# Optimization experiments

Hardware: AMD Instinct MI355X
Metric: run time of the kernel (lower is better)

Reference implementation:

```python
import jax, jax.numpy as jnp
import numpy as np
import math

V, E, R, B, T, L = 32000, 256, 1024, 64, 2048, 3
EPS = 1e-5


def setup_inputs() -> dict:
    key = jax.random.key(0)
    ks = jax.random.split(key, 8)
    x = jax.random.randint(ks[0], (B, T), 0, V)
    embed_w = jax.random.normal(ks[1], (V, E), jnp.float32)
    Win0 = jax.random.normal(ks[2], (E, R), jnp.float32) / math.sqrt(E) / 0.9
    Win1 = jax.random.normal(ks[3], (R, R), jnp.float32) / math.sqrt(R) / 0.9
    Win2 = jax.random.normal(ks[4], (R, R), jnp.float32) / math.sqrt(R) / 0.9
    R0 = jax.random.normal(ks[5], (R, R), jnp.float32) / math.sqrt(R) / 0.9
    R1 = jax.random.normal(ks[6], (R, R), jnp.float32) / math.sqrt(R) / 0.9
    R2 = jax.random.normal(ks[7], (R, R), jnp.float32) / math.sqrt(R) / 0.9
    ln_w = jnp.ones((R,), jnp.float32)
    ln_b = jnp.zeros((R,), jnp.float32)
    return dict(x=x, embed_w=embed_w, Win0=Win0, Win1=Win1, Win2=Win2,
                R0=R0, R1=R1, R2=R2, ln_w=ln_w, ln_b=ln_b)


def reference(x, embed_w, Win0, Win1, Win2, R0, R1, R2, ln_w, ln_b):
    Wins = (Win0, Win1, Win2)
    Rs = (R0, R1, R2)
    x_embed = embed_w[x]                        # [B, T, E]
    b = x.shape[0]
    rsz = R0.shape[0]
    init = tuple(jnp.zeros((b, rsz), x_embed.dtype) for _ in range(L))

    def step(states, xt):                       # xt: [B, E]
        cur = xt
        new = []
        for i in range(L):                      # 'deep': layer i>0 consumes states[i-1] (fresh)
            s = jnp.tanh(states[i] @ Rs[i] + cur @ Wins[i])
            new.append(s)
            cur = s
        return tuple(new), None

    states, _ = jax.lax.scan(step, init, jnp.swapaxes(x_embed, 0, 1))  # scan over T
    h = states[-1]                              # [B, R]
    mu = jnp.mean(h, axis=-1, keepdims=True)
    var = jnp.var(h, axis=-1, keepdims=True)
    return (h - mu) / jnp.sqrt(var + EPS) * ln_w + ln_b
```

## Files before the change

### kernel.cpp

```cpp
#include <hip/hip_runtime.h>

#define VV    32000
#define EE    256
#define RSZ   1024
#define BB    64
#define TT    2048
#define NGRP  3
#define EPSLN 1e-5f

#define NBLK_PER_GRP 64
#define NBLK  (NBLK_PER_GRP * NGRP)
#define NTHR  512
#define SLAB  (BB * RSZ)

#define BAR_OFF (NGRP * 2 * SLAB)

__device__ __forceinline__ void fma_step4x4(const float4 (&b)[4], const float* wrow,
                                            float (&acc)[4][4]) {
#pragma unroll
    for (int j = 0; j < 4; ++j) {
        const float4 w = *reinterpret_cast<const float4*>(wrow + j * 16);
#pragma unroll
        for (int r = 0; r < 4; ++r) {
            const float a = reinterpret_cast<const float*>(&b[r])[j];
            acc[r][0] = fmaf(a, w.x, acc[r][0]);
            acc[r][1] = fmaf(a, w.y, acc[r][1]);
            acc[r][2] = fmaf(a, w.z, acc[r][2]);
            acc[r][3] = fmaf(a, w.w, acc[r][3]);
        }
    }
}

template<int NSTEPS>
__device__ __forceinline__ void dot_stream(const float* const (&p)[4],
                                           const float* w, float (&acc)[4][4]) {
    float4 ring[4][4];
    constexpr int PRO = (NSTEPS < 4) ? NSTEPS : 4;
#pragma unroll
    for (int s = 0; s < PRO; ++s)
#pragma unroll
        for (int r = 0; r < 4; ++r)
            ring[s][r] = *reinterpret_cast<const float4*>(p[r] + s * 4);

    constexpr int MAIN = NSTEPS - PRO;
#pragma unroll
    for (int j = 0; j < MAIN; ++j) {
        fma_step4x4(ring[j & 3], w + j * 64, acc);
#pragma unroll
        for (int r = 0; r < 4; ++r)
            ring[j & 3][r] = *reinterpret_cast<const float4*>(p[r] + (j + 4) * 4);
    }
#pragma unroll
    for (int j = MAIN; j < NSTEPS; ++j)
        fma_step4x4(ring[j & 3], w + j * 64, acc);
}

__global__ __launch_bounds__(NTHR, 2)
void reservoir_main(const int*   __restrict__ x,
                    const float* __restrict__ embed_w,
                    const float* __restrict__ Win0,
                    const float* __restrict__ Win1,
                    const float* __restrict__ Win2,
                    const float* __restrict__ Rm0,
                    const float* __restrict__ Rm1,
                    const float* __restrict__ Rm2,
                    const float* __restrict__ ln_w,
                    const float* __restrict__ ln_b,
                    float*       __restrict__ states,
                    unsigned*    __restrict__ bar,
                    float*       __restrict__ out)
{
    const int blk   = blockIdx.x;
    const int grp   = blk >> 6;
    const int gb    = blk & 63;
    const int c0    = gb << 4;
    const int tid   = threadIdx.x;
    const int kg    = tid >> 6;
    const int idx   = tid & 63;
    const int rbase = (idx >> 2) << 2;
    const int cg4   = (idx & 3) << 2;

    const float* Wl  = (grp == 0) ? Win0 : ((grp == 1) ? Win1 : Win2);
    const float* Rl  = (grp == 0) ? Rm0  : ((grp == 1) ? Rm1  : Rm2);
    const int    Kw  = (grp == 0) ? EE : RSZ;
    const int    Kw8 = Kw >> 3;

    __shared__ float wlds[2048 * 16];
    __shared__ float pbuf[8][32][20];

    for (int i = tid; i < RSZ * 16; i += NTHR) {
        const int k = i >> 4, c = i & 15;
        wlds[i] = Rl[(size_t)k * RSZ + c0 + c];
    }
    for (int i = tid; i < Kw * 16; i += NTHR) {
        const int k = i >> 4, c = i & 15;
        wlds[RSZ * 16 + i] = Wl[(size_t)k * RSZ + c0 + c];
    }
    __syncthreads();

    unsigned* leaf  = bar;
    unsigned* root  = bar + 128;
    unsigned* epoch = bar + 160;

    float* const sl = states + (size_t)grp * 2 * SLAB;
    const float* const wRb = wlds + (kg << 7) * 16 + cg4;
    const float* const wWb = wlds + (RSZ + kg * Kw8) * 16 + cg4;

    int xidx[4];
    if (grp == 0) {
#pragma unroll
        for (int r = 0; r < 4; ++r) xidx[r] = x[(rbase + r) * TT + 0];
    }

    for (int tick = 0; tick < TT + NGRP - 1; ++tick) {
        const int t = tick - grp;
        if (0 <= t && t < TT) {
            const float* sprev = sl + (size_t)((t + 1) & 1) * SLAB;

            float acc[4][4];
#pragma unroll
            for (int r = 0; r < 4; ++r)
#pragma unroll
                for (int c = 0; c < 4; ++c) acc[r][c] = 0.f;

            {
                const float* aR[4];
#pragma unroll
                for (int r = 0; r < 4; ++r)
                    aR[r] = sprev + (size_t)(rbase + r) * RSZ + (kg << 7);
                dot_stream<32>(aR, wRb, acc);
            }
            {
                const float* aW[4];
                if (grp == 0) {
#pragma unroll
                    for (int r = 0; r < 4; ++r)
                        aW[r] = embed_w + (size_t)xidx[r] * EE + kg * Kw8;
                    dot_stream<8>(aW, wWb, acc);
                } else {
                    const float* cb = states + ((size_t)(grp - 1) * 2 + (t & 1)) * SLAB;
#pragma unroll
                    for (int r = 0; r < 4; ++r)
                        aW[r] = cb + (size_t)(rbase + r) * RSZ + kg * Kw8;
                    dot_stream<32>(aW, wWb, acc);
                }
            }

            if (grp == 0 && t + 1 < TT) {
#pragma unroll
                for (int r = 0; r < 4; ++r) xidx[r] = x[(rbase + r) * TT + t + 1];
            }

            float* sout = sl + (size_t)(t & 1) * SLAB;

            if (idx < 32) {
#pragma unroll
                for (int r = 0; r < 4; ++r) {
                    const int row = rbase + r;
                    *reinterpret_cast<float4*>(&pbuf[kg][row][cg4 ^ ((row & 3) << 2)])
                        = make_float4(acc[r][0], acc[r][1], acc[r][2], acc[r][3]);
                }
            }
            __syncthreads();
            {
                const int row = tid >> 4, col = tid & 15;
                const int cw  = ((col & 12) ^ ((row & 3) << 2)) | (col & 3);
                float s = 0.f;
#pragma unroll
                for (int g = 0; g < 8; ++g) s += pbuf[g][row][cw];
                sout[(size_t)row * RSZ + c0 + col] = tanhf(s);
            }
            __syncthreads();
            if (idx >= 32) {
#pragma unroll
                for (int r = 0; r < 4; ++r) {
                    const int row = rbase + r, rl = row & 31;
                    *reinterpret_cast<float4*>(&pbuf[kg][rl][cg4 ^ ((rl & 3) << 2)])
                        = make_float4(acc[r][0], acc[r][1], acc[r][2], acc[r][3]);
                }
            }
            __syncthreads();
            {
                const int rl = tid >> 4, col = tid & 15;
                const int cw = ((col & 12) ^ ((rl & 3) << 2)) | (col & 3);
                float s = 0.f;
#pragma unroll
                for (int g = 0; g < 8; ++g) s += pbuf[g][rl][cw];
                sout[(size_t)(32 + rl) * RSZ + c0 + col] = tanhf(s);
            }
        }

        __syncthreads();
        if (tid == 0) {
            __threadfence();
            const unsigned target = (unsigned)(tick + 1);
            unsigned prev = atomicAdd(&leaf[(blk & 7) << 4], 1u);
            if (prev == 24u * target - 1u) {
                prev = atomicAdd(root, 1u);
                if (prev == 8u * target - 1u)
                    __hip_atomic_store(epoch, target, __ATOMIC_RELEASE,
                                       __HIP_MEMORY_SCOPE_AGENT);
            }
            while (__hip_atomic_load(epoch, __ATOMIC_RELAXED,
                                     __HIP_MEMORY_SCOPE_AGENT) < target)
                __builtin_amdgcn_s_sleep(2);
            __threadfence();
        }
        __syncthreads();
    }

    if (blk < BB) {
        const float* h = states + ((size_t)2 * 2 + 1) * SLAB + (size_t)blk * RSZ;
        float* red = &pbuf[0][0][0];

        const float hv0 = h[tid];
        const float hv1 = h[tid + 512];
        float v = hv0 + hv1;
#pragma unroll
        for (int o = 32; o > 0; o >>= 1) v += __shfl_down(v, o, 64);
        if ((tid & 63) == 0) red[tid >> 6] = v;
        __syncthreads();
        if (tid == 0) {
            float s = 0.f;
#pragma unroll
            for (int i = 0; i < 8; ++i) s += red[i];
            red[20] = s / (float)RSZ;
        }
        __syncthreads();
        const float mu = red[20];
        const float d0 = hv0 - mu, d1 = hv1 - mu;
        v = d0 * d0 + d1 * d1;
#pragma unroll
        for (int o = 32; o > 0; o >>= 1) v += __shfl_down(v, o, 64);
        __syncthreads();
        if ((tid & 63) == 0) red[tid >> 6] = v;
        __syncthreads();
        if (tid == 0) {
            float s = 0.f;
#pragma unroll
            for (int i = 0; i < 8; ++i) s += red[i];
            red[21] = rsqrtf(s / (float)RSZ + EPSLN);
        }
        __syncthreads();
        const float inv = red[21];
        out[blk * RSZ + tid]       = d0 * inv * ln_w[tid]       + ln_b[tid];
        out[blk * RSZ + tid + 512] = d1 * inv * ln_w[tid + 512] + ln_b[tid + 512];
    }
}

extern "C" void kernel_launch(void* const* d_in, const int* in_sizes, int n_in,
                              void* d_out, int out_size, void* d_ws, size_t ws_size,
                              hipStream_t stream) {
    const int*   x       = (const int*)  d_in[0];
    const float* embed_w = (const float*)d_in[1];
    const float* Win0    = (const float*)d_in[2];
    const float* Win1    = (const float*)d_in[3];
    const float* Win2    = (const float*)d_in[4];
    const float* Rm0     = (const float*)d_in[5];
    const float* Rm1     = (const float*)d_in[6];
    const float* Rm2     = (const float*)d_in[7];
    const float* ln_w    = (const float*)d_in[8];
    const float* ln_b    = (const float*)d_in[9];
    float*       out     = (float*)d_out;
    float*       states  = (float*)d_ws;
    unsigned*    bar     = (unsigned*)((float*)d_ws + BAR_OFF);

    hipMemsetAsync(d_ws, 0, (size_t)BAR_OFF * sizeof(float) + 4096, stream);

    void* args[] = {
        (void*)&x, (void*)&embed_w,
        (void*)&Win0, (void*)&Win1, (void*)&Win2,
        (void*)&Rm0, (void*)&Rm1, (void*)&Rm2,
        (void*)&ln_w, (void*)&ln_b,
        (void*)&states, (void*)&bar, (void*)&out
    };
    hipLaunchCooperativeKernel(reinterpret_cast<void*>(reservoir_main),
                               dim3(NBLK), dim3(NTHR), args, 0, stream);
}
```

Measured before the change: 61.33 ms.

## Stage state rows into LDS via async global_load_lds triple-buffered pipeline

Replaces the per-thread register-ring global loads of previous-state and input rows with asynchronous global_load_lds copies into a triple-buffered, swizzled LDS staging area, with barriers between chunks. It also changes the thread mapping: 4 k-groups by 2 row-halves with 2 rows per thread, instead of 8 k-groups with 4 rows per thread. Each row chunk is then loaded once per block and shared across waves, which cuts redundant global/L2 traffic. The cost is a workgroup barrier per 32-wide chunk, plus more LDS use that may affect the two-blocks-per-CU occupancy.

```diff
diff --git a/kernel.cpp b/kernel.cpp
--- a/kernel.cpp
+++ b/kernel.cpp
@@ -15,45 +15,15 @@
 
 #define BAR_OFF (NGRP * 2 * SLAB)
 
-__device__ __forceinline__ void fma_step4x4(const float4 (&b)[4], const float* wrow,
-                                            float (&acc)[4][4]) {
-#pragma unroll
-    for (int j = 0; j < 4; ++j) {
-        const float4 w = *reinterpret_cast<const float4*>(wrow + j * 16);
-#pragma unroll
-        for (int r = 0; r < 4; ++r) {
-            const float a = reinterpret_cast<const float*>(&b[r])[j];
-            acc[r][0] = fmaf(a, w.x, acc[r][0]);
-            acc[r][1] = fmaf(a, w.y, acc[r][1]);
-            acc[r][2] = fmaf(a, w.z, acc[r][2]);
-            acc[r][3] = fmaf(a, w.w, acc[r][3]);
-        }
-    }
-}
-
-template<int NSTEPS>
-__device__ __forceinline__ void dot_stream(const float* const (&p)[4],
-                                           const float* w, float (&acc)[4][4]) {
-    float4 ring[4][4];
-    constexpr int PRO = (NSTEPS < 4) ? NSTEPS : 4;
-#pragma unroll
-    for (int s = 0; s < PRO; ++s)
-#pragma unroll
-        for (int r = 0; r < 4; ++r)
-            ring[s][r] = *reinterpret_cast<const float4*>(p[r] + s * 4);
-
-    constexpr int MAIN = NSTEPS - PRO;
-#pragma unroll
-    for (int j = 0; j < MAIN; ++j) {
-        fma_step4x4(ring[j & 3], w + j * 64, acc);
-#pragma unroll
-        for (int r = 0; r < 4; ++r)
-            ring[j & 3][r] = *reinterpret_cast<const float4*>(p[r] + (j + 4) * 4);
-    }
-#pragma unroll
-    for (int j = MAIN; j < NSTEPS; ++j)
-        fma_step4x4(ring[j & 3], w + j * 64, acc);
-}
+#define WOFF   0
+#define STAGE  (2048 * 16)
+#define CHUNKF (64 * 32)
+#define SMEMF  (STAGE + 3 * CHUNKF)
+
+typedef __attribute__((address_space(1))) const void gas_cvoid;
+typedef __attribute__((address_space(3))) void las_void;
+
+#define SCHED_FENCE() asm volatile("" ::: "memory")
 
 __global__ __launch_bounds__(NTHR, 2)
 void reservoir_main(const int*   __restrict__ x,
@@ -70,31 +40,39 @@
                     unsigned*    __restrict__ bar,
                     float*       __restrict__ out)
 {
-    const int blk   = blockIdx.x;
-    const int grp   = blk >> 6;
-    const int gb    = blk & 63;
-    const int c0    = gb << 4;
-    const int tid   = threadIdx.x;
-    const int kg    = tid >> 6;
-    const int idx   = tid & 63;
-    const int rbase = (idx >> 2) << 2;
-    const int cg4   = (idx & 3) << 2;
-
-    const float* Wl  = (grp == 0) ? Win0 : ((grp == 1) ? Win1 : Win2);
-    const float* Rl  = (grp == 0) ? Rm0  : ((grp == 1) ? Rm1  : Rm2);
-    const int    Kw  = (grp == 0) ? EE : RSZ;
-    const int    Kw8 = Kw >> 3;
-
-    __shared__ float wlds[2048 * 16];
-    __shared__ float pbuf[8][32][20];
+    const int blk  = blockIdx.x;
+    const int grp  = blk >> 6;
+    const int gb   = blk & 63;
+    const int c0   = gb << 4;
+    const int tid  = threadIdx.x;
+    const int wv   = tid >> 6;
+    const int lane = tid & 63;
+    const int kg   = wv & 3;
+    const int rh   = wv >> 2;
+    const int row0 = (rh << 5) + ((lane >> 2) << 1);
+    const int row1 = row0 + 1;
+    const int cg4  = (lane & 3) << 2;
+    const int sw0  = (row0 >> 1) & 7;
+    const int sw1  = (row1 >> 1) & 7;
+
+    const int srow = (wv << 3) + (lane >> 3);
+    const int sko  = lane & 7;
+    const int sswz = ((sko ^ ((srow >> 1) & 7)) << 2);
+
+    const float* Wl = (grp == 0) ? Win0 : ((grp == 1) ? Win1 : Win2);
+    const float* Rl = (grp == 0) ? Rm0  : ((grp == 1) ? Rm1  : Rm2);
+    const int Kw    = (grp == 0) ? EE : RSZ;
+    const int nCh   = 32 + (Kw >> 5);
+
+    __shared__ float smem[SMEMF];
 
     for (int i = tid; i < RSZ * 16; i += NTHR) {
         const int k = i >> 4, c = i & 15;
-        wlds[i] = Rl[(size_t)k * RSZ + c0 + c];
+        smem[WOFF + i] = Rl[(size_t)k * RSZ + c0 + c];
     }
     for (int i = tid; i < Kw * 16; i += NTHR) {
         const int k = i >> 4, c = i & 15;
-        wlds[RSZ * 16 + i] = Wl[(size_t)k * RSZ + c0 + c];
+        smem[WOFF + RSZ * 16 + i] = Wl[(size_t)k * RSZ + c0 + c];
     }
     __syncthreads();
 
@@ -103,89 +81,105 @@
     unsigned* epoch = bar + 160;
 
     float* const sl = states + (size_t)grp * 2 * SLAB;
-    const float* const wRb = wlds + (kg << 7) * 16 + cg4;
-    const float* const wWb = wlds + (RSZ + kg * Kw8) * 16 + cg4;
-
-    int xidx[4];
-    if (grp == 0) {
-#pragma unroll
-        for (int r = 0; r < 4; ++r) xidx[r] = x[(rbase + r) * TT + 0];
-    }
 
     for (int tick = 0; tick < TT + NGRP - 1; ++tick) {
         const int t = tick - grp;
         if (0 <= t && t < TT) {
             const float* sprev = sl + (size_t)((t + 1) & 1) * SLAB;
-
-            float acc[4][4];
-#pragma unroll
-            for (int r = 0; r < 4; ++r)
-#pragma unroll
-                for (int c = 0; c < 4; ++c) acc[r][c] = 0.f;
-
-            {
-                const float* aR[4];
-#pragma unroll
-                for (int r = 0; r < 4; ++r)
-                    aR[r] = sprev + (size_t)(rbase + r) * RSZ + (kg << 7);
-                dot_stream<32>(aR, wRb, acc);
-            }
-            {
-                const float* aW[4];
-                if (grp == 0) {
-#pragma unroll
-                    for (int r = 0; r < 4; ++r)
-                        aW[r] = embed_w + (size_t)xidx[r] * EE + kg * Kw8;
-                    dot_stream<8>(aW, wWb, acc);
-                } else {
-                    const float* cb = states + ((size_t)(grp - 1) * 2 + (t & 1)) * SLAB;
-#pragma unroll
-                    for (int r = 0; r < 4; ++r)
-                        aW[r] = cb + (size_t)(rbase + r) * RSZ + kg * Kw8;
-                    dot_stream<32>(aW, wWb, acc);
+            const float* gR = sprev + (size_t)srow * RSZ + sswz;
+            const float* gW;
+            if (grp == 0) {
+                const int tok = x[srow * TT + t];
+                gW = embed_w + (size_t)tok * EE + sswz;
+            } else {
+                gW = states + ((size_t)(grp - 1) * 2 + (t & 1)) * SLAB
+                     + (size_t)srow * RSZ + sswz;
+            }
+            asm volatile("s_waitcnt vmcnt(0)" ::: "memory");
+
+            float acc[2][4] = {{0.f,0.f,0.f,0.f},{0.f,0.f,0.f,0.f}};
+
+            auto ISSUE = [&](int c) {
+                const float* g = (c < 32) ? (gR + (c << 5)) : (gW + ((c - 32) << 5));
+                float* l = &smem[STAGE + (c % 3) * CHUNKF + (wv << 8)];
+                __builtin_amdgcn_global_load_lds((gas_cvoid*)g, (las_void*)l, 16, 0, 0);
+            };
+            auto COMPUTE = [&](int c) {
+                const int sb = STAGE + (c % 3) * CHUNKF;
+                const int wk = (c < 32) ? (c << 5) : (RSZ + ((c - 32) << 5));
+                const int wb = WOFF + (wk + (kg << 3)) * 16 + cg4;
+#pragma unroll
+                for (int s = 0; s < 2; ++s) {
+                    const int kol = (kg << 1) + s;
+                    const float4 a0 = *(const float4*)&smem[sb + row0 * 32 + ((kol ^ sw0) << 2)];
+                    const float4 a1 = *(const float4*)&smem[sb + row1 * 32 + ((kol ^ sw1) << 2)];
+#pragma unroll
+                    for (int j = 0; j < 4; ++j) {
+                        const float4 w = *(const float4*)&smem[wb + ((s << 2) + j) * 16];
+                        const float e0 = ((const float*)&a0)[j];
+                        const float e1 = ((const float*)&a1)[j];
+                        acc[0][0] = fmaf(e0, w.x, acc[0][0]);
+                        acc[0][1] = fmaf(e0, w.y, acc[0][1]);
+                        acc[0][2] = fmaf(e0, w.z, acc[0][2]);
+                        acc[0][3] = fmaf(e0, w.w, acc[0][3]);
+                        acc[1][0] = fmaf(e1, w.x, acc[1][0]);
+                        acc[1][1] = fmaf(e1, w.y, acc[1][1]);
+                        acc[1][2] = fmaf(e1, w.z, acc[1][2]);
+                        acc[1][3] = fmaf(e1, w.w, acc[1][3]);
+                    }
                 }
-            }
-
-            if (grp == 0 && t + 1 < TT) {
-#pragma unroll
-                for (int r = 0; r < 4; ++r) xidx[r] = x[(rbase + r) * TT + t + 1];
+            };
+
+            ISSUE(0);
+            ISSUE(1);
+            asm volatile("s_waitcnt vmcnt(1)" ::: "memory");
+            __builtin_amdgcn_s_barrier();
+            SCHED_FENCE();
+
+            for (int c = 0; c < nCh; ++c) {
+                if (c + 2 < nCh) ISSUE(c + 2);
+                COMPUTE(c);
+                if (c + 2 < nCh) {
+                    asm volatile("s_waitcnt vmcnt(1)" ::: "memory");
+                } else if (c + 1 < nCh) {
+                    asm volatile("s_waitcnt vmcnt(0)" ::: "memory");
+                }
+                __builtin_amdgcn_s_barrier();
+                SCHED_FENCE();
             }
 
             float* sout = sl + (size_t)(t & 1) * SLAB;
 
-            if (idx < 32) {
-#pragma unroll
-                for (int r = 0; r < 4; ++r) {
-                    const int row = rbase + r;
-                    *reinterpret_cast<float4*>(&pbuf[kg][row][cg4 ^ ((row & 3) << 2)])
-                        = make_float4(acc[r][0], acc[r][1], acc[r][2], acc[r][3]);
-                }
+            if (wv < 4) {
+                *(float4*)&smem[STAGE + ((kg << 5) + row0) * 20 + (cg4 ^ ((row0 & 3) << 2))]
+                    = make_float4(acc[0][0], acc[0][1], acc[0][2], acc[0][3]);
+                *(float4*)&smem[STAGE + ((kg << 5) + row1) * 20 + (cg4 ^ ((row1 & 3) << 2))]
+                    = make_float4(acc[1][0], acc[1][1], acc[1][2], acc[1][3]);
             }
             __syncthreads();
             {
                 const int row = tid >> 4, col = tid & 15;
-                const int cw  = ((col & 12) ^ ((row & 3) << 2)) | (col & 3);
+                const int cw  = (((col & 12) ^ ((row & 3) << 2)) | (col & 3));
                 float s = 0.f;
 #pragma unroll
-                for (int g = 0; g < 8; ++g) s += pbuf[g][row][cw];
+                for (int g = 0; g < 4; ++g) s += smem[STAGE + ((g << 5) + row) * 20 + cw];
                 sout[(size_t)row * RSZ + c0 + col] = tanhf(s);
             }
             __syncthreads();
-            if (idx >= 32) {
-#pragma unroll
-                for (int r = 0; r < 4; ++r) {
-                    const int row = rbase + r, rl = row & 31;
-                    *reinterpret_cast<float4*>(&pbuf[kg][rl][cg4 ^ ((rl & 3) << 2)])
-                        = make_float4(acc[r][0], acc[r][1], acc[r][2], acc[r][3]);
-                }
+            if (wv >= 4) {
+                const int rl0 = row0 & 31, rl1 = row1 & 31;
+                *(float4*)&smem[STAGE + ((kg << 5) + rl0) * 20 + (cg4 ^ ((rl0 & 3) << 2))]
+                    = make_float4(acc[0][0], acc[0][1], acc[0][2], acc[0][3]);
+                *(float4*)&smem[STAGE + ((kg << 5) + rl1) * 20 + (cg4 ^ ((rl1 & 3) << 2))]
+                    = make_float4(acc[1][0], acc[1][1], acc[1][2], acc[1][3]);
             }
             __syncthreads();
             {
                 const int rl = tid >> 4, col = tid & 15;
-                const int cw = ((col & 12) ^ ((rl & 3) << 2)) | (col & 3);
+                const int cw = (((col & 12) ^ ((rl & 3) << 2)) | (col & 3));
                 float s = 0.f;
 #pragma unroll
-                for (int g = 0; g < 8; ++g) s += pbuf[g][rl][cw];
+                for (int g = 0; g < 4; ++g) s += smem[STAGE + ((g << 5) + rl) * 20 + cw];
                 sout[(size_t)(32 + rl) * RSZ + c0 + col] = tanhf(s);
             }
         }
@@ -211,7 +205,7 @@
 
     if (blk < BB) {
         const float* h = states + ((size_t)2 * 2 + 1) * SLAB + (size_t)blk * RSZ;
-        float* red = &pbuf[0][0][0];
+        float* red = &smem[STAGE];
 
         const float hv0 = h[tid];
         const float hv1 = h[tid + 512];
```

Result: slower. 89.96 ms (+46.7%).

## Use 8x4 register tiles with 16-way K split and double-buffered loads

Applied to the files above, without the earlier changes.

Each thread now computes 8 batch rows by 4 columns over a K slice half as long, split 16 ways instead of 8. This doubles reuse of each LDS weight float4 across rows and replaces the 4-deep load ring with a two-buffer A/B scheme. The partial-sum reduction now runs in four 16-row phases with 16 partials each, and launch bounds drop to one block per SM to leave room for the extra registers. The cost is more barriers per step, a longer reduction, and a risk of register pressure or stalls from less load pipelining.

```diff
diff --git a/kernel.cpp b/kernel.cpp
--- a/kernel.cpp
+++ b/kernel.cpp
@@ -15,13 +15,13 @@
 
 #define BAR_OFF (NGRP * 2 * SLAB)
 
-__device__ __forceinline__ void fma_step4x4(const float4 (&b)[4], const float* wrow,
-                                            float (&acc)[4][4]) {
+__device__ __forceinline__ void fma_step8x4(const float4 (&b)[8], const float* wrow,
+                                            float (&acc)[8][4]) {
 #pragma unroll
     for (int j = 0; j < 4; ++j) {
         const float4 w = *reinterpret_cast<const float4*>(wrow + j * 16);
 #pragma unroll
-        for (int r = 0; r < 4; ++r) {
+        for (int r = 0; r < 8; ++r) {
             const float a = reinterpret_cast<const float*>(&b[r])[j];
             acc[r][0] = fmaf(a, w.x, acc[r][0]);
             acc[r][1] = fmaf(a, w.y, acc[r][1]);
@@ -31,31 +31,30 @@
     }
 }
 
+__device__ __forceinline__ void ld8(float4 (&b)[8], const float* const (&p)[8],
+                                    int off) {
+#pragma unroll
+    for (int r = 0; r < 8; ++r)
+        b[r] = *reinterpret_cast<const float4*>(p[r] + off);
+}
+
 template<int NSTEPS>
-__device__ __forceinline__ void dot_stream(const float* const (&p)[4],
-                                           const float* w, float (&acc)[4][4]) {
-    float4 ring[4][4];
-    constexpr int PRO = (NSTEPS < 4) ? NSTEPS : 4;
-#pragma unroll
-    for (int s = 0; s < PRO; ++s)
-#pragma unroll
-        for (int r = 0; r < 4; ++r)
-            ring[s][r] = *reinterpret_cast<const float4*>(p[r] + s * 4);
-
-    constexpr int MAIN = NSTEPS - PRO;
-#pragma unroll
-    for (int j = 0; j < MAIN; ++j) {
-        fma_step4x4(ring[j & 3], w + j * 64, acc);
-#pragma unroll
-        for (int r = 0; r < 4; ++r)
-            ring[j & 3][r] = *reinterpret_cast<const float4*>(p[r] + (j + 4) * 4);
-    }
-#pragma unroll
-    for (int j = MAIN; j < NSTEPS; ++j)
-        fma_step4x4(ring[j & 3], w + j * 64, acc);
-}
-
-__global__ __launch_bounds__(NTHR, 2)
+__device__ __forceinline__ void dot8(const float* const (&p)[8],
+                                     const float* w, float (&acc)[8][4]) {
+    float4 A[8], B[8];
+    ld8(A, p, 0);
+    ld8(B, p, 4);
+    for (int j = 0; j < NSTEPS - 2; j += 2) {
+        fma_step8x4(A, w + j * 64, acc);
+        ld8(A, p, (j + 2) * 4);
+        fma_step8x4(B, w + (j + 1) * 64, acc);
+        ld8(B, p, (j + 3) * 4);
+    }
+    fma_step8x4(A, w + (NSTEPS - 2) * 64, acc);
+    fma_step8x4(B, w + (NSTEPS - 1) * 64, acc);
+}
+
+__global__ __launch_bounds__(NTHR, 1)
 void reservoir_main(const int*   __restrict__ x,
                     const float* __restrict__ embed_w,
                     const float* __restrict__ Win0,
@@ -75,18 +74,19 @@
     const int gb    = blk & 63;
     const int c0    = gb << 4;
     const int tid   = threadIdx.x;
-    const int kg    = tid >> 6;
-    const int idx   = tid & 63;
-    const int rbase = (idx >> 2) << 2;
+    const int kg    = tid >> 5;
+    const int idx   = tid & 31;
+    const int rbase = (idx >> 2) << 3;
     const int cg4   = (idx & 3) << 2;
+    const int ph    = rbase >> 4;
 
     const float* Wl  = (grp == 0) ? Win0 : ((grp == 1) ? Win1 : Win2);
     const float* Rl  = (grp == 0) ? Rm0  : ((grp == 1) ? Rm1  : Rm2);
     const int    Kw  = (grp == 0) ? EE : RSZ;
-    const int    Kw8 = Kw >> 3;
+    const int    KwS = Kw >> 4;
 
     __shared__ float wlds[2048 * 16];
-    __shared__ float pbuf[8][32][20];
+    __shared__ float pbuf[16][16][20];
 
     for (int i = tid; i < RSZ * 16; i += NTHR) {
         const int k = i >> 4, c = i & 15;
@@ -103,13 +103,13 @@
     unsigned* epoch = bar + 160;
 
     float* const sl = states + (size_t)grp * 2 * SLAB;
-    const float* const wRb = wlds + (kg << 7) * 16 + cg4;
-    const float* const wWb = wlds + (RSZ + kg * Kw8) * 16 + cg4;
-
-    int xidx[4];
+    const float* const wRb = wlds + (kg << 6) * 16 + cg4;
+    const float* const wWb = wlds + (RSZ + kg * KwS) * 16 + cg4;
+
+    int xidx[8];
     if (grp == 0) {
 #pragma unroll
-        for (int r = 0; r < 4; ++r) xidx[r] = x[(rbase + r) * TT + 0];
+        for (int r = 0; r < 8; ++r) xidx[r] = x[(rbase + r) * TT + 0];
     }
 
     for (int tick = 0; tick < TT + NGRP - 1; ++tick) {
@@ -117,76 +117,62 @@
         if (0 <= t && t < TT) {
             const float* sprev = sl + (size_t)((t + 1) & 1) * SLAB;
 
-            float acc[4][4];
-#pragma unroll
-            for (int r = 0; r < 4; ++r)
+            float acc[8][4];
+#pragma unroll
+            for (int r = 0; r < 8; ++r)
 #pragma unroll
                 for (int c = 0; c < 4; ++c) acc[r][c] = 0.f;
 
             {
-                const float* aR[4];
-#pragma unroll
-                for (int r = 0; r < 4; ++r)
-                    aR[r] = sprev + (size_t)(rbase + r) * RSZ + (kg << 7);
-                dot_stream<32>(aR, wRb, acc);
+                const float* aR[8];
+#pragma unroll
+                for (int r = 0; r < 8; ++r)
+                    aR[r] = sprev + (size_t)(rbase + r) * RSZ + (kg << 6);
+                dot8<16>(aR, wRb, acc);
             }
             {
-                const float* aW[4];
+                const float* aW[8];
                 if (grp == 0) {
 #pragma unroll
-                    for (int r = 0; r < 4; ++r)
-                        aW[r] = embed_w + (size_t)xidx[r] * EE + kg * Kw8;
-                    dot_stream<8>(aW, wWb, acc);
+                    for (int r = 0; r < 8; ++r)
+                        aW[r] = embed_w + (size_t)xidx[r] * EE + kg * KwS;
+                    dot8<4>(aW, wWb, acc);
                 } else {
                     const float* cb = states + ((size_t)(grp - 1) * 2 + (t & 1)) * SLAB;
 #pragma unroll
-                    for (int r = 0; r < 4; ++r)
-                        aW[r] = cb + (size_t)(rbase + r) * RSZ + kg * Kw8;
-                    dot_stream<32>(aW, wWb, acc);
+                    for (int r = 0; r < 8; ++r)
+                        aW[r] = cb + (size_t)(rbase + r) * RSZ + kg * KwS;
+                    dot8<16>(aW, wWb, acc);
                 }
             }
 
             if (grp == 0 && t + 1 < TT) {
 #pragma unroll
-                for (int r = 0; r < 4; ++r) xidx[r] = x[(rbase + r) * TT + t + 1];
+                for (int r = 0; r < 8; ++r) xidx[r] = x[(rbase + r) * TT + t + 1];
             }
 
             float* sout = sl + (size_t)(t & 1) * SLAB;
-
-            if (idx < 32) {
-#pragma unroll
-                for (int r = 0; r < 4; ++r) {
-                    const int row = rbase + r;
-                    *reinterpret_cast<float4*>(&pbuf[kg][row][cg4 ^ ((row & 3) << 2)])
-                        = make_float4(acc[r][0], acc[r][1], acc[r][2], acc[r][3]);
+#pragma unroll
+            for (int p = 0; p < 4; ++p) {
+                if (ph == p) {
+#pragma unroll
+                    for (int r = 0; r < 8; ++r) {
+                        const int lr = (rbase + r) & 15;
+                        *reinterpret_cast<float4*>(
+                            &pbuf[kg][lr][cg4 ^ ((lr & 3) << 2)])
+                            = make_float4(acc[r][0], acc[r][1], acc[r][2], acc[r][3]);
+                    }
                 }
-            }
-            __syncthreads();
-            {
-                const int row = tid >> 4, col = tid & 15;
-                const int cw  = ((col & 12) ^ ((row & 3) << 2)) | (col & 3);
-                float s = 0.f;
-#pragma unroll
-                for (int g = 0; g < 8; ++g) s += pbuf[g][row][cw];
-                sout[(size_t)row * RSZ + c0 + col] = tanhf(s);
-            }
-            __syncthreads();
-            if (idx >= 32) {
-#pragma unroll
-                for (int r = 0; r < 4; ++r) {
-                    const int row = rbase + r, rl = row & 31;
-                    *reinterpret_cast<float4*>(&pbuf[kg][rl][cg4 ^ ((rl & 3) << 2)])
-                        = make_float4(acc[r][0], acc[r][1], acc[r][2], acc[r][3]);
+                __syncthreads();
+                if (tid < 256) {
+                    const int rl = tid >> 4, col = tid & 15;
+                    const int cw = ((col & 12) ^ ((rl & 3) << 2)) | (col & 3);
+                    float s = 0.f;
+#pragma unroll
+                    for (int g = 0; g < 16; ++g) s += pbuf[g][rl][cw];
+                    sout[(size_t)(16 * p + rl) * RSZ + c0 + col] = tanhf(s);
                 }
-            }
-            __syncthreads();
-            {
-                const int rl = tid >> 4, col = tid & 15;
-                const int cw = ((col & 12) ^ ((rl & 3) << 2)) | (col & 3);
-                float s = 0.f;
-#pragma unroll
-                for (int g = 0; g < 8; ++g) s += pbuf[g][rl][cw];
-                sout[(size_t)(32 + rl) * RSZ + c0 + col] = tanhf(s);
+                __syncthreads();
             }
         }
 
```

Measured after the change: 63.82 ms. 4.1% more time.
